# Performance work log

Measured on AMD Instinct MI355X. Metric: run time of the kernel, lower is better.

Reference implementation:

```python
import jax, jax.numpy as jnp
import numpy as np
from jax import lax

SUR_BETA = 4.0
THRESH = 1.0
ALPHA = float(np.exp(-1.0 / 20.0))  # membrane decay, tau_mem=20
BETA = float(np.exp(-1.0 / 5.0))    # synaptic decay, tau_syn=5

@jax.custom_vjp
def spike(x):
    return (x >= 0).astype(jnp.float32)

def _spike_fwd(x):
    return spike(x), x

def _spike_bwd(x, g):
    e = jnp.exp(-SUR_BETA * jnp.abs(x))
    sg = SUR_BETA * e / (2.0 * (1.0 + e) ** 2)
    return (g * sg,)

spike.defvjp(_spike_fwd, _spike_bwd)

def lif_layer(x, W, b):
    # x: [B, T, Din] -> spikes [B, T, H]
    xt = jnp.einsum('bti,ih->bth', x, W) + b
    B, T, H = xt.shape
    z = jnp.zeros((B, H), xt.dtype)
    def step(carry, x_t):
        v, i = carry
        i = BETA * i + x_t
        v = ALPHA * v + i
        s = spike(v - THRESH)
        v = v * (1.0 - s)  # multiplicative reset
        return (v, i), s
    _, sp = lax.scan(step, (z, z), xt.transpose(1, 0, 2))
    return sp.transpose(1, 0, 2)

def layer_norm(x, scale, bias, eps=1e-6):
    m = jnp.mean(x, axis=-1, keepdims=True)
    v = jnp.mean((x - m) ** 2, axis=-1, keepdims=True)
    return (x - m) / jnp.sqrt(v + eps) * scale + bias

def setup_inputs() -> dict:
    key = jax.random.key(0)
    ks = jax.random.split(key, 6)
    B, T, S, F = 64, 512, 64, 16
    D = S * F  # 1024
    def w(k, shape, fan):
        return (jax.random.normal(k, shape, jnp.float32) / np.sqrt(fan)).astype(jnp.float32)
    return dict(
        spike_trains=(jax.random.uniform(ks[0], (B, T, S, F)) < 0.2).astype(jnp.float32),
        W0=w(ks[1], (D, 256), D), b0=jnp.zeros((256,), jnp.float32),
        W1=w(ks[2], (256, 128), 256), b1=jnp.zeros((128,), jnp.float32),
        W2=w(ks[3], (128, 64), 128), b2=jnp.zeros((64,), jnp.float32),
        ln1_scale=jnp.ones((256,), jnp.float32), ln1_bias=jnp.zeros((256,), jnp.float32),
        ln2_scale=jnp.ones((128,), jnp.float32), ln2_bias=jnp.zeros((128,), jnp.float32),
        Wc=w(ks[4], (B, 2), B), bc=jnp.zeros((2,), jnp.float32),
    )

def reference(spike_trains, W0, b0, W1, b1, W2, b2,
              ln1_scale, ln1_bias, ln2_scale, ln2_bias, Wc, bc):
    B, T, S, F = spike_trains.shape
    x = spike_trains.reshape(B, T, S * F)
    x = lif_layer(x, W0, b0)                                   # [B,T,256]
    x = lif_layer(layer_norm(x, ln1_scale, ln1_bias), W1, b1)  # [B,T,128]
    x = lif_layer(layer_norm(x, ln2_scale, ln2_bias), W2, b2)  # [B,T,64]
    pooled = jnp.mean(x, axis=(1, 2))  # [B]  (faithful to source: mean over time AND hidden)
    logits = pooled @ Wc + bc          # [num_classes] -- classifier sees batch as feature dim
    return (logits, pooled, jnp.mean(x))
```

## Files before the change

### kernel.cpp

```cpp
#include <hip/hip_runtime.h>

#define T_STEPS 512
#define BATCH 64

__device__ constexpr float ALPHA_ = 0.95122942450071400910f;
__device__ constexpr float BETA_  = 0.81873075307798185867f;

typedef __attribute__((ext_vector_type(8))) short bf16x8;
typedef __attribute__((ext_vector_type(4))) float f32x4;

__device__ inline unsigned short f2bf_rne(float f) {
  union { float f; unsigned int u; } v{f};
  const unsigned int u = v.u;
  return (unsigned short)((u + 0x7FFFu + ((u >> 16) & 1u)) >> 16);
}
__device__ inline float bf2f(unsigned short h) {
  union { unsigned int u; float f; } v{(unsigned int)h << 16};
  return v.f;
}

__device__ inline void gload16(const void* g, void* l) {
  __builtin_amdgcn_global_load_lds(
      (const __attribute__((address_space(1))) unsigned int*)g,
      (__attribute__((address_space(3))) unsigned int*)l, 16, 0, 0);
}

__device__ inline unsigned int pkbf(float first, float second) {
#if __has_builtin(__builtin_amdgcn_perm)
  return __builtin_amdgcn_perm(__float_as_uint(second), __float_as_uint(first),
                               0x07060302u);
#else
  return (__float_as_uint(first) >> 16) | (__float_as_uint(second) & 0xFFFF0000u);
#endif
}

__device__ inline bf16x8 cvt_frag(const f32x4 lo, const f32x4 hi) {
  union { unsigned int w[4]; bf16x8 v; } u;
  u.w[0] = pkbf(lo.x, lo.y);
  u.w[1] = pkbf(lo.z, lo.w);
  u.w[2] = pkbf(hi.x, hi.y);
  u.w[3] = pkbf(hi.z, hi.w);
  return u.v;
}

#define SB __builtin_amdgcn_sched_barrier(0)

template <int WM, int WC, int TM, bool A_F32, bool LNFOLD, bool COAL>
__global__ __launch_bounds__(256) void gemm_deep2(
    const void* __restrict__ Av, const char* __restrict__ Bhi,
    const char* __restrict__ Blo, const float* __restrict__ uvec,
    const float* __restrict__ cvec, float* __restrict__ C, int N, int K) {
  constexpr int BM = WM * TM;
  constexpr int FM = TM / 16;
  constexpr int ABY = A_F32 ? BM * 128 : BM * 64;
  constexpr int AIP = ABY / 4096;
  constexpr int ASTEP = A_F32 ? 128 : 64;
  constexpr int W2N = AIP + 16;
  __shared__ char smem[3 * ABY];

  const int tid = threadIdx.x;
  const int lane = tid & 63;
  const int wave = tid >> 6;
  const int wm = wave / WC, wc = wave % WC;
  const int l15 = lane & 15, l4 = lane >> 4;
  const int row0 = blockIdx.y * BM;
  const int col0 = blockIdx.x * (WC * 64);
  const int KB = K / 32;

  const char* Ab = (const char*)Av;

  const char* a_src[AIP];
#pragma unroll
  for (int i = 0; i < AIP; ++i) {
    const int unit = i * 256 + tid;
    if constexpr (A_F32 && COAL) {
      const int r = unit >> 3, c = unit & 7;
      a_src[i] = Ab + ((size_t)(row0 + r) * K) * 4 + ((c * 16) ^ ((r & 7) << 4));
    } else if constexpr (A_F32) {
      const int fr = unit >> 7, h = (unit >> 6) & 1, ln = unit & 63;
      a_src[i] = Ab + ((size_t)(row0 + fr * 16 + (ln & 15)) * K + ((ln >> 4) * 8)) * 4 + h * 16;
    } else {
      const int r = ((unit >> 6) << 4) | (unit & 15);
      const int j = (unit >> 4) & 3;
      a_src[i] = Ab + ((size_t)(row0 + r) * K + j * 8) * 2;
    }
  }
  const char* bh_base = Bhi + (size_t)(blockIdx.x * WC + wc) * KB * 4096 + (size_t)lane * 16;
  const char* bl_base = Blo + (size_t)(blockIdx.x * WC + wc) * KB * 4096 + (size_t)lane * 16;

  int aoff = 0, boff = 0;
  const int amax = (KB - 1) * ASTEP;
  const int bmax = (KB - 1) * 4096;

  f32x4 acc[FM][4] = {};
  f32x4 acc1[FM] = {};
  const bf16x8 ONES = {0x3F80, 0x3F80, 0x3F80, 0x3F80,
                       0x3F80, 0x3F80, 0x3F80, 0x3F80};
  bf16x8 bh0[4], bl0[4], bh1[4], bl1[4];

#define STAGE_A(buf)                                                   \
  do {                                                                 \
    _Pragma("unroll") for (int i = 0; i < AIP; ++i)                    \
        gload16(a_src[i] + aoff, (buf) + (i * 256 + tid) * 16);        \
  } while (0)

#define LOAD_B(bh, bl, off_)                                           \
  do {                                                                 \
    const char* ph = bh_base + (off_);                                 \
    const char* pl = bl_base + (off_);                                 \
    bh[0] = *(const bf16x8*)(ph);                                      \
    bh[1] = *(const bf16x8*)(ph + 1024);                               \
    bh[2] = *(const bf16x8*)(ph + 2048);                               \
    bh[3] = *(const bf16x8*)(ph + 3072);                               \
    bl[0] = *(const bf16x8*)(pl);                                      \
    bl[1] = *(const bf16x8*)(pl + 1024);                               \
    bl[2] = *(const bf16x8*)(pl + 2048);                               \
    bl[3] = *(const bf16x8*)(pl + 3072);                               \
  } while (0)

  char* bufR = smem;
  char* bufM = smem + ABY;
  char* bufS = smem + 2 * ABY;

  SB;
  STAGE_A(bufR);
  SB;
  LOAD_B(bh0, bl0, 0);
  SB;
  aoff = ASTEP;
  STAGE_A(bufM);
  SB;
  LOAD_B(bh1, bl1, 4096);
  SB;
  aoff = (2 * ASTEP < amax) ? 2 * ASTEP : amax;
  boff = (2 * 4096 < bmax) ? 2 * 4096 : bmax;
  asm volatile("s_waitcnt vmcnt(%0)" ::"i"(W2N) : "memory");
  __builtin_amdgcn_s_barrier();
  SB;

#define KSTEP(BH, BL)                                                        \
  do {                                                                       \
    STAGE_A(bufS);                                              \
    aoff = (aoff < amax) ? aoff + ASTEP : aoff;                              \
    SB;                                                                      \
    bf16x8 af[FM];                                                           \
    _Pragma("unroll") for (int m = 0; m < FM; ++m) {                         \
      if constexpr (A_F32 && COAL) {                                         \
        const int rr = wm * TM + m * 16 + l15;                               \
        const int sw = (rr & 7) << 4;                                        \
        const f32x4 lo = *(const f32x4*)(bufR + rr * 128 + ((l4 * 32) ^ sw)); \
        const f32x4 hi = *(const f32x4*)(bufR + rr * 128 + ((l4 * 32 + 16) ^ sw)); \
        af[m] = cvt_frag(lo, hi);                                            \
      } else if constexpr (A_F32) {                                          \
        const int fr = wm * FM + m;                                          \
        const f32x4 lo = *(const f32x4*)(bufR + ((fr * 2 + 0) * 64 + lane) * 16); \
        const f32x4 hi = *(const f32x4*)(bufR + ((fr * 2 + 1) * 64 + lane) * 16); \
        af[m] = cvt_frag(lo, hi);                                            \
      } else {                                                               \
        const int fr = wm * FM + m;                                          \
        af[m] = *(const bf16x8*)(bufR + (fr * 64 + lane) * 16);              \
      }                                                                      \
    }                                                                        \
    SB;                                                                      \
    _Pragma("unroll") for (int m = 0; m < FM; ++m) {                         \
      _Pragma("unroll") for (int n = 0; n < 4; ++n) {                        \
        acc[m][n] = __builtin_amdgcn_mfma_f32_16x16x32_bf16(af[m], BH[n],    \
                                                            acc[m][n], 0, 0, 0); \
        acc[m][n] = __builtin_amdgcn_mfma_f32_16x16x32_bf16(af[m], BL[n],    \
                                                            acc[m][n], 0, 0, 0); \
      }                                                                      \
      if constexpr (LNFOLD)                                                  \
        acc1[m] = __builtin_amdgcn_mfma_f32_16x16x32_bf16(af[m], ONES,       \
                                                          acc1[m], 0, 0, 0); \
    }                                                                        \
    SB;                                                                      \
    LOAD_B(BH, BL, boff);                                       \
    boff = (boff < bmax) ? boff + 4096 : boff;                               \
    SB;                                                                      \
    asm volatile("s_waitcnt vmcnt(%0)" ::"i"(W2N) : "memory");               \
    __builtin_amdgcn_s_barrier();                                            \
    SB;                                                                      \
    { char* t = bufR; bufR = bufM; bufM = bufS; bufS = t; }                  \
  } while (0)

  const int ITER = KB / 2;
  for (int it = 0; it < ITER; ++it) {
    KSTEP(bh0, bl0);
    KSTEP(bh1, bl1);
  }
  asm volatile("s_waitcnt vmcnt(0) lgkmcnt(0)" ::: "memory");

#undef KSTEP
#undef LOAD_B
#undef STAGE_A

  const int row0w = row0 + wm * TM;
  const int col0w = col0 + wc * 64;
#pragma unroll
  for (int m = 0; m < FM; ++m) {
    const int rbase = row0w + m * 16 + l4 * 4;
    float iv[4], mv[4];
    if constexpr (LNFOLD) {
#pragma unroll
      for (int r = 0; r < 4; ++r) {
        const float mean = acc1[m][r] / (float)K;
        const float inv = 1.0f / sqrtf(mean * (1.f - mean) + 1e-6f);
        iv[r] = inv;
        mv[r] = mean * inv;
      }
    }
#pragma unroll
    for (int n = 0; n < 4; ++n) {
      const int c = col0w + n * 16 + l15;
      const float cc = cvec[c];
      float uu = 0.f;
      if constexpr (LNFOLD) uu = uvec[c];
#pragma unroll
      for (int r = 0; r < 4; ++r) {
        float v;
        if constexpr (LNFOLD) v = iv[r] * acc[m][n][r] - mv[r] * uu + cc;
        else v = acc[m][n][r] + cc;
        C[(size_t)(rbase + r) * N + c] = v;
      }
    }
  }
}

__global__ void prep_split(const float* __restrict__ W, const float* __restrict__ s,
                           char* __restrict__ hi, char* __restrict__ lo,
                           int K, int N) {
  const int g = blockIdx.x * 256 + threadIdx.x;
  const int total = (K * N) / 8;
  if (g >= total) return;
  constexpr int UB = 256;
  const int KB = K / 32;
  const int unit = g % UB;
  const int kb = (g / UB) % KB;
  const int cb = g / (UB * KB);
  const int n = cb * 64 + ((unit >> 6) << 4) + (unit & 15);
  const int kbase = kb * 32 + ((unit >> 4) & 3) * 8;
  short h8[8], l8[8];
#pragma unroll
  for (int jj = 0; jj < 8; ++jj) {
    const int k = kbase + jj;
    float w = W[(size_t)k * N + n];
    if (s) w *= s[k];
    const unsigned short hb = f2bf_rne(w);
    const unsigned short lb = f2bf_rne(w - bf2f(hb));
    h8[jj] = (short)hb;
    l8[jj] = (short)lb;
  }
  *(bf16x8*)(hi + (size_t)g * 16) = *(const bf16x8*)h8;
  *(bf16x8*)(lo + (size_t)g * 16) = *(const bf16x8*)l8;
}

__global__ __launch_bounds__(256) void prep_consts(
    const float* __restrict__ W, const float* __restrict__ s,
    const float* __restrict__ b, const float* __restrict__ bias2,
    float* __restrict__ u, float* __restrict__ c, int K, int N) {
  const int n = blockIdx.x;
  const int t = threadIdx.x;
  float us = 0.f, cs = 0.f;
  for (int k = t; k < K; k += 256) {
    const float w = W[(size_t)k * N + n];
    us += s[k] * w;
    cs += b[k] * w;
  }
  __shared__ float su[256], sc[256];
  su[t] = us;
  sc[t] = cs;
  __syncthreads();
  for (int o = 128; o > 0; o >>= 1) {
    if (t < o) { su[t] += su[t + o]; sc[t] += sc[t + o]; }
    __syncthreads();
  }
  if (t == 0) { u[n] = su[0]; c[n] = sc[0] + bias2[n]; }
}

template <int H, bool SPIKE_OUT, bool ACCUM>
__global__ void lif_scan(const float* __restrict__ xt,
                         unsigned short* __restrict__ sp,
                         float* __restrict__ tsum) {
  const int n = blockIdx.x * 64 + threadIdx.x;
  const int b = n / H, h = n % H;
  const float* p = xt + (size_t)b * T_STEPS * H + h;
  unsigned short* q = nullptr;
  if constexpr (SPIKE_OUT) q = sp + (size_t)b * T_STEPS * H + h;

  float v = 0.f, cur = 0.f, ts = 0.f;
  for (int t = 0; t < T_STEPS; t += 128) {
    float x[128];
#pragma unroll
    for (int u = 0; u < 128; ++u) x[u] = p[(size_t)u * H];
#pragma unroll
    for (int u = 0; u < 128; ++u) {
      cur = BETA_ * cur + x[u];
      v = ALPHA_ * v + cur;
      const bool sb = (v >= 1.f);
      if constexpr (SPIKE_OUT) q[(size_t)u * H] = sb ? 0x3F80 : 0;
      if constexpr (ACCUM) ts += sb ? 1.f : 0.f;
      v = sb ? 0.f : v;
    }
    p += (size_t)128 * H;
    if constexpr (SPIKE_OUT) q += (size_t)128 * H;
  }
  if constexpr (ACCUM) tsum[n] = ts;
}

__global__ void finalize(const float* __restrict__ tsum,
                         const float* __restrict__ Wc,
                         const float* __restrict__ bc,
                         float* __restrict__ out) {
  const int b = threadIdx.x;
  float s = 0.f;
#pragma unroll 8
  for (int h = 0; h < 64; ++h) s += tsum[b * 64 + h];
  const float pooled = s * (1.0f / (512.f * 64.f));
  out[2 + b] = pooled;

  float tot = pooled;
  float l0 = pooled * Wc[b * 2 + 0];
  float l1 = pooled * Wc[b * 2 + 1];
#pragma unroll
  for (int off = 32; off > 0; off >>= 1) {
    tot += __shfl_xor(tot, off);
    l0 += __shfl_xor(l0, off);
    l1 += __shfl_xor(l1, off);
  }
  if (b == 0) {
    out[0] = l0 + bc[0];
    out[1] = l1 + bc[1];
    out[66] = tot * (1.0f / 64.f);
  }
}

extern "C" void kernel_launch(void* const* d_in, const int* in_sizes, int n_in,
                              void* d_out, int out_size, void* d_ws, size_t ws_size,
                              hipStream_t stream) {
  const float* X    = (const float*)d_in[0];
  const float* W0   = (const float*)d_in[1];
  const float* b0   = (const float*)d_in[2];
  const float* W1   = (const float*)d_in[3];
  const float* b1   = (const float*)d_in[4];
  const float* W2   = (const float*)d_in[5];
  const float* b2   = (const float*)d_in[6];
  const float* ln1s = (const float*)d_in[7];
  const float* ln1b = (const float*)d_in[8];
  const float* ln2s = (const float*)d_in[9];
  const float* ln2b = (const float*)d_in[10];
  const float* Wc   = (const float*)d_in[11];
  const float* bc   = (const float*)d_in[12];
  float* out = (float*)d_out;

  char* w = (char*)d_ws;
  float* buf0 = (float*)w;
  float* buf1 = (float*)w;
  float* buf2 = (float*)(w + 16777216);
  size_t off = 33554432;
  unsigned short* sp0 = (unsigned short*)(w + off); off += 16777216;
  unsigned short* sp1 = (unsigned short*)(w + off); off += 8388608;
  char* hi0 = w + off; off += 524288;
  char* lo0 = w + off; off += 524288;
  char* hi1 = w + off; off += 65536;
  char* lo1 = w + off; off += 65536;
  char* hi2 = w + off; off += 16384;
  char* lo2 = w + off; off += 16384;
  float* u1 = (float*)(w + off); off += 512;
  float* c1 = (float*)(w + off); off += 512;
  float* u2 = (float*)(w + off); off += 256;
  float* c2 = (float*)(w + off); off += 256;
  float* tsum = (float*)(w + off); off += 16384;

  const int M = 32768;

  prep_split<<<128, 256, 0, stream>>>(W0, nullptr, hi0, lo0, 1024, 256);
  prep_split<<<16, 256, 0, stream>>>(W1, ln1s, hi1, lo1, 256, 128);
  prep_split<<<4, 256, 0, stream>>>(W2, ln2s, hi2, lo2, 128, 64);
  prep_consts<<<128, 256, 0, stream>>>(W1, ln1s, ln1b, b1, u1, c1, 256, 128);
  prep_consts<<<64, 256, 0, stream>>>(W2, ln2s, ln2b, b2, u2, c2, 128, 64);

  gemm_deep2<1, 4, 64, true, false, true><<<dim3(1, M / 64), 256, 0, stream>>>(
      X, hi0, lo0, nullptr, b0, buf0, 256, 1024);
  lif_scan<256, true, false><<<(BATCH * 256) / 64, 64, 0, stream>>>(buf0, sp0, nullptr);

  gemm_deep2<2, 2, 32, false, true, false><<<dim3(1, M / 64), 256, 0, stream>>>(
      sp0, hi1, lo1, u1, c1, buf1, 128, 256);
  lif_scan<128, true, false><<<(BATCH * 128) / 64, 64, 0, stream>>>(buf1, sp1, nullptr);

  gemm_deep2<4, 1, 32, false, true, false><<<dim3(1, M / 128), 256, 0, stream>>>(
      sp1, hi2, lo2, u2, c2, buf2, 64, 128);
  lif_scan<64, false, true><<<(BATCH * 64) / 64, 64, 0, stream>>>(buf2, nullptr, tsum);

  finalize<<<1, 64, 0, stream>>>(tsum, Wc, bc, out);
}
```

Before: 125.3 us.

## Load fp32 A operand directly to registers and stage B in LDS for layer-0 GEMM

Adds a new layer-0 GEMM kernel that reads the fp32 input rows straight from global memory into registers, double-buffered across k-steps, and converts them to bf16 in-register. The split hi/lo weights are staged through a triple-buffered LDS ring instead. The grid now splits the 256 output columns across two blocks of 128 columns. This is meant to cut LDS traffic and footprint for the large fp32 A tile, but each A row is now fetched by both column blocks and the per-lane global loads are strided. The old fp32-A code paths in the generic kernel are removed.

Result: slower. 174.5 us (+39.3%).

```diff
diff --git a/kernel.cpp b/kernel.cpp
--- a/kernel.cpp
+++ b/kernel.cpp
@@ -45,16 +45,139 @@
 
 #define SB __builtin_amdgcn_sched_barrier(0)
 
-template <int WM, int WC, int TM, bool A_F32, bool LNFOLD, bool COAL>
+__global__ __launch_bounds__(256) void gemm_areg(
+    const float* __restrict__ A, const char* __restrict__ Bhi,
+    const char* __restrict__ Blo, const float* __restrict__ cvec,
+    float* __restrict__ C, int N, int K) {
+  __shared__ char Bbuf[3][16384];
+
+  const int tid = threadIdx.x;
+  const int lane = tid & 63;
+  const int wave = tid >> 6;
+  const int wm = wave >> 1, wc = wave & 1;
+  const int l15 = lane & 15, l4 = lane >> 4;
+  const int row0 = blockIdx.y * 64;
+  const int col0 = blockIdx.x * 128;
+  const int KB = K / 32;
+
+  const float* a_base[2];
+#pragma unroll
+  for (int m = 0; m < 2; ++m)
+    a_base[m] = A + (size_t)(row0 + wm * 32 + m * 16 + l15) * K + l4 * 8;
+
+  const char* bh_src[2];
+  const char* bl_src[2];
+#pragma unroll
+  for (int i = 0; i < 2; ++i) {
+    const int u = i * 256 + tid;
+    const int g = u >> 8, inner = u & 255;
+    const size_t so = ((size_t)(blockIdx.x * 2 + g) * KB) * 4096 + (size_t)inner * 16;
+    bh_src[i] = Bhi + so;
+    bl_src[i] = Blo + so;
+  }
+
+  int boff = 0;
+  const int bmax = (KB - 1) * 4096;
+  int aoff = 0;
+  const int amax = (KB - 1) * 32;
+
+  f32x4 acc[2][4] = {};
+  f32x4 aLo0[2], aHi0[2], aLo1[2], aHi1[2];
+
+#define STAGE_B(buf)                                                    \
+  do {                                                                  \
+    _Pragma("unroll") for (int i = 0; i < 2; ++i) {                     \
+      gload16(bh_src[i] + boff, (buf) + (i * 256 + tid) * 16);          \
+      gload16(bl_src[i] + boff, (buf) + 8192 + (i * 256 + tid) * 16);   \
+    }                                                                   \
+  } while (0)
+
+#define LOAD_A(lo_, hi_)                                                \
+  do {                                                                  \
+    _Pragma("unroll") for (int m = 0; m < 2; ++m) {                     \
+      lo_[m] = *(const f32x4*)(a_base[m] + aoff);                       \
+      hi_[m] = *(const f32x4*)(a_base[m] + aoff + 4);                   \
+    }                                                                   \
+  } while (0)
+
+  SB;
+  STAGE_B(Bbuf[0]);
+  SB;
+  LOAD_A(aLo0, aHi0);
+  SB;
+  boff = 4096;
+  STAGE_B(Bbuf[1]);
+  SB;
+  boff = (2 * 4096 < bmax) ? 2 * 4096 : bmax;
+  aoff = (32 < amax) ? 32 : amax;
+  asm volatile("s_waitcnt vmcnt(8)" ::: "memory");
+  __builtin_amdgcn_s_barrier();
+  SB;
+
+#define KSTEP(ALOC, AHIC, ALON, AHIN, BUFC, BUFN2)                           \
+  do {                                                                       \
+    LOAD_A(ALON, AHIN);                                         \
+    aoff = (aoff < amax) ? aoff + 32 : aoff;                                 \
+    SB;                                                                      \
+    STAGE_B(BUFN2);                                             \
+    boff = (boff < bmax) ? boff + 4096 : boff;                               \
+    SB;                                                                      \
+    bf16x8 af[2], bh[4], bl[4];                                              \
+    _Pragma("unroll") for (int m = 0; m < 2; ++m)                            \
+        af[m] = cvt_frag(ALOC[m], AHIC[m]);                                  \
+    _Pragma("unroll") for (int n = 0; n < 4; ++n) {                          \
+      bh[n] = *(const bf16x8*)((BUFC) + ((wc * 256 + n * 64 + lane)) * 16);  \
+      bl[n] = *(const bf16x8*)((BUFC) + 8192 + ((wc * 256 + n * 64 + lane)) * 16); \
+    }                                                                        \
+    _Pragma("unroll") for (int m = 0; m < 2; ++m)                            \
+      _Pragma("unroll") for (int n = 0; n < 4; ++n) {                        \
+        acc[m][n] = __builtin_amdgcn_mfma_f32_16x16x32_bf16(af[m], bh[n],    \
+                                                            acc[m][n], 0, 0, 0); \
+        acc[m][n] = __builtin_amdgcn_mfma_f32_16x16x32_bf16(af[m], bl[n],    \
+                                                            acc[m][n], 0, 0, 0); \
+      }                                                                      \
+    SB;                                                                      \
+    asm volatile("s_waitcnt vmcnt(8)" ::: "memory");     \
+    __builtin_amdgcn_s_barrier();                                            \
+    SB;                                                                      \
+  } while (0)
+
+  const int ITER = KB / 2;
+  for (int it = 0; it < ITER; ++it) {
+    const int kb = it * 2;
+    KSTEP(aLo0, aHi0, aLo1, aHi1, Bbuf[kb % 3], Bbuf[(kb + 2) % 3]);
+    KSTEP(aLo1, aHi1, aLo0, aHi0, Bbuf[(kb + 1) % 3], Bbuf[(kb + 3) % 3]);
+  }
+  asm volatile("s_waitcnt vmcnt(0) lgkmcnt(0)" ::: "memory");
+
+#undef KSTEP
+#undef LOAD_A
+#undef STAGE_B
+
+#pragma unroll
+  for (int m = 0; m < 2; ++m) {
+    const int rbase = row0 + wm * 32 + m * 16 + l4 * 4;
+#pragma unroll
+    for (int n = 0; n < 4; ++n) {
+      const int c = col0 + wc * 64 + n * 16 + l15;
+      const float cc = cvec[c];
+#pragma unroll
+      for (int r = 0; r < 4; ++r)
+        C[(size_t)(rbase + r) * N + c] = acc[m][n][r] + cc;
+    }
+  }
+}
+
+template <int WM, int WC, int TM, bool LNFOLD>
 __global__ __launch_bounds__(256) void gemm_deep2(
     const void* __restrict__ Av, const char* __restrict__ Bhi,
     const char* __restrict__ Blo, const float* __restrict__ uvec,
     const float* __restrict__ cvec, float* __restrict__ C, int N, int K) {
   constexpr int BM = WM * TM;
   constexpr int FM = TM / 16;
-  constexpr int ABY = A_F32 ? BM * 128 : BM * 64;
+  constexpr int ABY = BM * 64;
   constexpr int AIP = ABY / 4096;
-  constexpr int ASTEP = A_F32 ? 128 : 64;
+  constexpr int ASTEP = 64;
   constexpr int W2N = AIP + 16;
   __shared__ char smem[3 * ABY];
 
@@ -73,17 +196,9 @@
 #pragma unroll
   for (int i = 0; i < AIP; ++i) {
     const int unit = i * 256 + tid;
-    if constexpr (A_F32 && COAL) {
-      const int r = unit >> 3, c = unit & 7;
-      a_src[i] = Ab + ((size_t)(row0 + r) * K) * 4 + ((c * 16) ^ ((r & 7) << 4));
-    } else if constexpr (A_F32) {
-      const int fr = unit >> 7, h = (unit >> 6) & 1, ln = unit & 63;
-      a_src[i] = Ab + ((size_t)(row0 + fr * 16 + (ln & 15)) * K + ((ln >> 4) * 8)) * 4 + h * 16;
-    } else {
-      const int r = ((unit >> 6) << 4) | (unit & 15);
-      const int j = (unit >> 4) & 3;
-      a_src[i] = Ab + ((size_t)(row0 + r) * K + j * 8) * 2;
-    }
+    const int r = ((unit >> 6) << 4) | (unit & 15);
+    const int j = (unit >> 4) & 3;
+    a_src[i] = Ab + ((size_t)(row0 + r) * K + j * 8) * 2;
   }
   const char* bh_base = Bhi + (size_t)(blockIdx.x * WC + wc) * KB * 4096 + (size_t)lane * 16;
   const char* bl_base = Blo + (size_t)(blockIdx.x * WC + wc) * KB * 4096 + (size_t)lane * 16;
@@ -140,26 +255,13 @@
 
 #define KSTEP(BH, BL)                                                        \
   do {                                                                       \
-    STAGE_A(bufS);                                              \
+    STAGE_A(bufS);                                                           \
     aoff = (aoff < amax) ? aoff + ASTEP : aoff;                              \
     SB;                                                                      \
     bf16x8 af[FM];                                                           \
     _Pragma("unroll") for (int m = 0; m < FM; ++m) {                         \
-      if constexpr (A_F32 && COAL) {                                         \
-        const int rr = wm * TM + m * 16 + l15;                               \
-        const int sw = (rr & 7) << 4;                                        \
-        const f32x4 lo = *(const f32x4*)(bufR + rr * 128 + ((l4 * 32) ^ sw)); \
-        const f32x4 hi = *(const f32x4*)(bufR + rr * 128 + ((l4 * 32 + 16) ^ sw)); \
-        af[m] = cvt_frag(lo, hi);                                            \
-      } else if constexpr (A_F32) {                                          \
-        const int fr = wm * FM + m;                                          \
-        const f32x4 lo = *(const f32x4*)(bufR + ((fr * 2 + 0) * 64 + lane) * 16); \
-        const f32x4 hi = *(const f32x4*)(bufR + ((fr * 2 + 1) * 64 + lane) * 16); \
-        af[m] = cvt_frag(lo, hi);                                            \
-      } else {                                                               \
-        const int fr = wm * FM + m;                                          \
-        af[m] = *(const bf16x8*)(bufR + (fr * 64 + lane) * 16);              \
-      }                                                                      \
+      const int fr = wm * FM + m;                                            \
+      af[m] = *(const bf16x8*)(bufR + (fr * 64 + lane) * 16);                \
     }                                                                        \
     SB;                                                                      \
     _Pragma("unroll") for (int m = 0; m < FM; ++m) {                         \
@@ -174,7 +276,7 @@
                                                           acc1[m], 0, 0, 0); \
     }                                                                        \
     SB;                                                                      \
-    LOAD_B(BH, BL, boff);                                       \
+    LOAD_B(BH, BL, boff);                                                    \
     boff = (boff < bmax) ? boff + 4096 : boff;                               \
     SB;                                                                      \
     asm volatile("s_waitcnt vmcnt(%0)" ::"i"(W2N) : "memory");               \
@@ -379,15 +481,15 @@
   prep_consts<<<128, 256, 0, stream>>>(W1, ln1s, ln1b, b1, u1, c1, 256, 128);
   prep_consts<<<64, 256, 0, stream>>>(W2, ln2s, ln2b, b2, u2, c2, 128, 64);
 
-  gemm_deep2<1, 4, 64, true, false, true><<<dim3(1, M / 64), 256, 0, stream>>>(
-      X, hi0, lo0, nullptr, b0, buf0, 256, 1024);
+  gemm_areg<<<dim3(2, M / 64), 256, 0, stream>>>(
+      X, hi0, lo0, b0, buf0, 256, 1024);
   lif_scan<256, true, false><<<(BATCH * 256) / 64, 64, 0, stream>>>(buf0, sp0, nullptr);
 
-  gemm_deep2<2, 2, 32, false, true, false><<<dim3(1, M / 64), 256, 0, stream>>>(
+  gemm_deep2<2, 2, 32, true><<<dim3(1, M / 64), 256, 0, stream>>>(
       sp0, hi1, lo1, u1, c1, buf1, 128, 256);
   lif_scan<128, true, false><<<(BATCH * 128) / 64, 64, 0, stream>>>(buf1, sp1, nullptr);
 
-  gemm_deep2<4, 1, 32, false, true, false><<<dim3(1, M / 128), 256, 0, stream>>>(
+  gemm_deep2<4, 1, 32, true><<<dim3(1, M / 128), 256, 0, stream>>>(
       sp1, hi2, lo2, u2, c2, buf2, 64, 128);
   lif_scan<64, false, true><<<(BATCH * 64) / 64, 64, 0, stream>>>(buf2, nullptr, tsum);
 
```
